# Optimization experiments

Hardware: AMD Instinct MI355X
Metric: run time of the kernel (lower is better)

The kernel has to match this reference:

```python
import jax, jax.numpy as jnp
import numpy as np

B, S, H, E, V = 64, 2048, 1024, 512, 32000


def setup_inputs() -> dict:
    key = jax.random.key(0)
    ks = jax.random.split(key, 10)
    s = lambda k, shape, scale: jax.random.normal(k, shape, jnp.float32) * scale
    return {
        "input_batch": jax.random.randint(ks[0], (B,), 0, V),
        "prev_h": s(ks[1], (B, H), 0.1),
        "prev_c": s(ks[2], (B, H), 0.1),
        "encoder_outputs": s(ks[3], (S, B, H), 0.1),
        "emb_W": s(ks[4], (V, E), 0.02),           # nn.Embedding weight
        "attn_W": s(ks[5], (2 * H,), 0.02),        # nn.Linear(2H, 1) weight (flattened)
        "attn_b": jnp.zeros((), jnp.float32),
        "W_ih": s(ks[6], (4 * H, E + H), 0.02),    # LSTMCell weight_ih
        "W_hh": s(ks[7], (4 * H, H), 0.02),        # LSTMCell weight_hh
        "b_ih": jnp.zeros((4 * H,), jnp.float32),
        "b_hh": jnp.zeros((4 * H,), jnp.float32),
        "out_W": s(ks[8], (V, H), 0.02),           # linear_out weight
        "out_b": jnp.zeros((V,), jnp.float32),
    }


def reference(input_batch, prev_h, prev_c, encoder_outputs, emb_W, attn_W, attn_b,
              W_ih, W_hh, b_ih, b_hh, out_W, out_b):
    hid = prev_h.shape[1]
    emb = emb_W[input_batch]                                   # [B, E]

    # Additive attention score attn(cat(prev_h[i], enc[j,i])) vectorized:
    # score[b, s] = prev_h[b] . W[:H] + enc[s, b] . W[H:] + bias
    Wh, We = attn_W[:hid], attn_W[hid:]
    scores = (prev_h @ Wh)[:, None] + jnp.einsum("sbh,h->bs", encoder_outputs, We) + attn_b
    attn_weights = jax.nn.softmax(scores, axis=1)              # [B, S]

    # context = bmm(attn[B,1,S], enc^T[B,S,H]) -> [B, H]
    context = jnp.einsum("bs,sbh->bh", attn_weights, encoder_outputs)

    x = jnp.concatenate([emb, context], axis=1)                # [B, E+H]

    # LSTMCell step (PyTorch gate order: i, f, g, o)
    gates = x @ W_ih.T + b_ih + prev_h @ W_hh.T + b_hh         # [B, 4H]
    i, f, g, o = jnp.split(gates, 4, axis=1)
    i, f, o = jax.nn.sigmoid(i), jax.nn.sigmoid(f), jax.nn.sigmoid(o)
    g = jnp.tanh(g)
    cell = f * prev_c + i * g
    hidden = o * jnp.tanh(cell)

    logits = hidden @ out_W.T + out_b                          # [B, V]
    output = jax.nn.log_softmax(logits, axis=1)
    return output, hidden, cell, attn_weights
```

## Files before the change

### kernel.cpp

```cpp
#include <hip/hip_runtime.h>
#include <math.h>

#define B 64
#define S 2048
#define H 1024
#define E 512
#define V 32000
#define G4 4096
#define KX 1536
#define KC 2560
#define NVT 500

typedef __attribute__((ext_vector_type(8))) short short8v;
typedef __attribute__((ext_vector_type(4))) float f32x4;

__device__ __forceinline__ ushort f2bf(float f) {
    union { float f; unsigned u; } v; v.f = f;
    unsigned r = v.u + 0x7FFFu + ((v.u >> 16) & 1u);
    return (ushort)(r >> 16);
}

__device__ __forceinline__ float4 ntload4(const float* p) {
    f32x4 v = __builtin_nontemporal_load((const f32x4*)p);
    return make_float4(v[0], v[1], v[2], v[3]);
}

__global__ __launch_bounds__(256) void prep_kernel(const int* __restrict__ ib,
                                                   const float* __restrict__ emb_W,
                                                   const float* __restrict__ prev_h,
                                                   const float* __restrict__ attn_W,
                                                   float* __restrict__ hwh,
                                                   float* __restrict__ xT) {
    __shared__ float red[256];
    int t = threadIdx.x;
    if (blockIdx.x < 64) {
        int b = blockIdx.x;
        float4 p = *(const float4*)(prev_h + b * H + t * 4);
        float4 w = *(const float4*)(attn_W + t * 4);
        red[t] = p.x * w.x + p.y * w.y + p.z * w.z + p.w * w.w;
        __syncthreads();
        for (int s2 = 128; s2; s2 >>= 1) {
            if (t < s2) red[t] += red[t + s2];
            __syncthreads();
        }
        if (t == 0) hwh[b] = red[0];
    } else {
        int g = (blockIdx.x - 64) * 256 + t;
        if (g < E * B) {
            int b = g & 63, k = g >> 6;
            xT[k * B + b] = emb_W[(size_t)ib[b] * E + k];
        } else {
            int g2 = g - E * B;
            int b = g2 & 63, k = g2 >> 6;
            xT[(KX + k) * B + b] = prev_h[b * H + k];
        }
    }
}

__global__ __launch_bounds__(256) void fused_attn_kernel(const float* __restrict__ enc,
                                                         const float* __restrict__ attn_W,
                                                         const float* __restrict__ attn_b,
                                                         const float* __restrict__ hwh,
                                                         float* __restrict__ scores,
                                                         float* __restrict__ cpart,
                                                         float* __restrict__ mlc) {
    __shared__ float mw[4], lw[4];
    __shared__ float cbuf[4][1024];
    int t = threadIdx.x;
    int lane = t & 63, wid = t >> 6;
    int bx = blockIdx.x;
    int b = bx >> 5, chunk = bx & 31;
    int s0 = chunk * 64 + wid * 16;

    const float* We = attn_W + H;
    float4 we4[4];
#pragma unroll
    for (int c = 0; c < 4; ++c) we4[c] = *(const float4*)(We + c * 256 + lane * 4);
    float cst = hwh[b] + attn_b[0];

    float m = -INFINITY, l = 0.f;
    float4 ctx4[4] = {{0,0,0,0},{0,0,0,0},{0,0,0,0},{0,0,0,0}};

    const float* rowp = enc + (size_t)s0 * (B * H) + b * H + lane * 4;
    float4 e4[4];
#pragma unroll
    for (int c = 0; c < 4; ++c) e4[c] = ntload4(rowp + c * 256);

    for (int i = 0; i < 16; ++i) {
        float4 cur[4];
#pragma unroll
        for (int c = 0; c < 4; ++c) cur[c] = e4[c];
        if (i < 15) {
            const float* np = rowp + (size_t)(i + 1) * (B * H);
#pragma unroll
            for (int c = 0; c < 4; ++c) e4[c] = ntload4(np + c * 256);
        }
        float acc = 0.f;
#pragma unroll
        for (int c = 0; c < 4; ++c)
            acc += cur[c].x * we4[c].x + cur[c].y * we4[c].y +
                   cur[c].z * we4[c].z + cur[c].w * we4[c].w;
#pragma unroll
        for (int x = 32; x; x >>= 1) acc += __shfl_xor(acc, x);
        float score = acc + cst;
        if (lane == 0) scores[b * S + s0 + i] = score;
        float nm = fmaxf(m, score);
        float sc = expf(m - nm);
        float w = expf(score - nm);
        l = l * sc + w;
        m = nm;
#pragma unroll
        for (int c = 0; c < 4; ++c) {
            ctx4[c].x = ctx4[c].x * sc + w * cur[c].x;
            ctx4[c].y = ctx4[c].y * sc + w * cur[c].y;
            ctx4[c].z = ctx4[c].z * sc + w * cur[c].z;
            ctx4[c].w = ctx4[c].w * sc + w * cur[c].w;
        }
    }

    if (lane == 0) { mw[wid] = m; lw[wid] = l; }
    __syncthreads();
    float M = fmaxf(fmaxf(mw[0], mw[1]), fmaxf(mw[2], mw[3]));
    float L = lw[0] * expf(mw[0] - M) + lw[1] * expf(mw[1] - M) +
              lw[2] * expf(mw[2] - M) + lw[3] * expf(mw[3] - M);
    float msc = expf(m - M);
#pragma unroll
    for (int c = 0; c < 4; ++c) {
        float4 v = ctx4[c];
        v.x *= msc; v.y *= msc; v.z *= msc; v.w *= msc;
        *(float4*)&cbuf[wid][c * 256 + lane * 4] = v;
    }
    __syncthreads();
    if (wid == 0) {
#pragma unroll
        for (int c = 0; c < 4; ++c) {
            int h = c * 256 + lane * 4;
            float4 a0 = *(float4*)&cbuf[0][h];
            float4 a1 = *(float4*)&cbuf[1][h];
            float4 a2 = *(float4*)&cbuf[2][h];
            float4 a3 = *(float4*)&cbuf[3][h];
            float4 s4 = make_float4(a0.x + a1.x + a2.x + a3.x,
                                    a0.y + a1.y + a2.y + a3.y,
                                    a0.z + a1.z + a2.z + a3.z,
                                    a0.w + a1.w + a2.w + a3.w);
            *(float4*)(cpart + (size_t)(chunk * B + b) * H + h) = s4;
        }
    }
    if (t == 0) {
        mlc[(b * 32 + chunk) * 2] = M;
        mlc[(b * 32 + chunk) * 2 + 1] = L;
    }
}

__global__ __launch_bounds__(256) void attn_reduce_kernel(const float* __restrict__ cpart,
                                                          const float* __restrict__ mlc,
                                                          const float* __restrict__ scores,
                                                          float* __restrict__ xT,
                                                          float* __restrict__ attn) {
    __shared__ float Ms[32], Ls[32], Es[32];
    int blk = blockIdx.x;
    int b = blk >> 2, q = blk & 3;
    int t = threadIdx.x;
    if (t < 32) {
        Ms[t] = mlc[(b * 32 + t) * 2];
        Ls[t] = mlc[(b * 32 + t) * 2 + 1];
    }
    __syncthreads();
    float Mg = -INFINITY;
#pragma unroll
    for (int c = 0; c < 32; ++c) Mg = fmaxf(Mg, Ms[c]);
    if (t < 32) Es[t] = expf(Ms[t] - Mg);
    __syncthreads();
    float Lg = 0.f;
#pragma unroll
    for (int c = 0; c < 32; ++c) Lg += Ls[c] * Es[c];
    float inv = 1.f / Lg;
    int h = q * 256 + t;
    float acc = 0.f;
#pragma unroll 4
    for (int c = 0; c < 32; ++c)
        acc += Es[c] * cpart[(size_t)(c * B + b) * H + h];
    xT[(E + h) * B + b] = acc * inv;
#pragma unroll
    for (int i = 0; i < 2; ++i) {
        int s = q * 512 + i * 256 + t;
        attn[b * S + s] = expf(scores[b * S + s] - Mg) * inv;
    }
}

__global__ __launch_bounds__(256) void gates_gemm(const float* __restrict__ W_ih,
                                                  const float* __restrict__ W_hh,
                                                  const float* __restrict__ xT,
                                                  float* __restrict__ gpart) {
    __shared__ float Wt[64][68];
    __shared__ float Xt[64][68];
    int t = threadIdx.x;
    int rtile = blockIdx.x >> 3, ks = blockIdx.x & 7;
    int r0 = rtile * 64;
    int rr0 = (t >> 4) * 4;
    int c0 = (t & 15) * 4;
    int sv = t >> 4;
    int sk = (t & 15) * 4;
    float acc[4][4] = {{0.f}};
    for (int kt = 0; kt < 5; ++kt) {
        int kb = ks * 320 + kt * 64;
        const float* wbase;
        int wstride;
        if (kb < KX) { wbase = W_ih + kb; wstride = KX; }
        else         { wbase = W_hh + (kb - KX); wstride = H; }
        __syncthreads();
#pragma unroll
        for (int g = 0; g < 4; ++g) {
            int vv = sv + g * 16;
            *(float4*)&Wt[vv][sk] = *(const float4*)(wbase + (size_t)(r0 + vv) * wstride + sk);
            *(float4*)&Xt[vv][sk] = *(const float4*)(xT + (size_t)(kb + vv) * B + sk);
        }
        __syncthreads();
#pragma unroll
        for (int k0 = 0; k0 < 64; k0 += 4) {
            float w[4][4], x[4][4];
#pragma unroll
            for (int ri = 0; ri < 4; ++ri) *(float4*)w[ri] = *(const float4*)&Wt[rr0 + ri][k0];
#pragma unroll
            for (int kj = 0; kj < 4; ++kj) *(float4*)x[kj] = *(const float4*)&Xt[k0 + kj][c0];
#pragma unroll
            for (int kj = 0; kj < 4; ++kj)
#pragma unroll
                for (int ri = 0; ri < 4; ++ri)
#pragma unroll
                    for (int ci = 0; ci < 4; ++ci)
                        acc[ri][ci] += w[ri][kj] * x[kj][ci];
        }
    }
#pragma unroll
    for (int ri = 0; ri < 4; ++ri) {
        float4 o4 = make_float4(acc[ri][0], acc[ri][1], acc[ri][2], acc[ri][3]);
        *(float4*)(gpart + (size_t)ks * (G4 * B) + (size_t)(r0 + rr0 + ri) * B + c0) = o4;
    }
}

__global__ __launch_bounds__(256) void lstm_kernel(const float* __restrict__ gpart,
                                                   const float* __restrict__ b_ih,
                                                   const float* __restrict__ b_hh,
                                                   const float* __restrict__ prev_c,
                                                   float* __restrict__ hidden_out,
                                                   float* __restrict__ cell_out,
                                                   ushort* __restrict__ hb) {
    int t = blockIdx.x * 256 + threadIdx.x;
    int b = t & 63, h = t >> 6;
    float g[4];
#pragma unroll
    for (int q = 0; q < 4; ++q) {
        int r = h + q * H;
        float a = b_ih[r] + b_hh[r];
#pragma unroll
        for (int ks = 0; ks < 8; ++ks) a += gpart[(size_t)ks * (G4 * B) + r * B + b];
        g[q] = a;
    }
    float ig = 1.f / (1.f + expf(-g[0]));
    float fg = 1.f / (1.f + expf(-g[1]));
    float gg = tanhf(g[2]);
    float og = 1.f / (1.f + expf(-g[3]));
    float c = fg * prev_c[b * H + h] + ig * gg;
    float hd = og * tanhf(c);
    cell_out[b * H + h] = c;
    hidden_out[b * H + h] = hd;
    hb[b * H + h] = f2bf(hd);
}

__global__ __launch_bounds__(256) void logits_mfma(const float* __restrict__ W,
                                                   const float* __restrict__ ob,
                                                   const ushort* __restrict__ hb,
                                                   float* __restrict__ outl,
                                                   float* __restrict__ lsp) {
    __shared__ ushort Wt[64 * 64];
    __shared__ ushort Bt[64 * 64];
    __shared__ float  Ct[64][68];
    int t = threadIdx.x;
    int lane = t & 63, wid = t >> 6;
    int v0 = blockIdx.x * 64;

    int srow = t >> 2;
    int sq = t & 3;

    f32x4 acc[4] = {{0.f,0.f,0.f,0.f},{0.f,0.f,0.f,0.f},{0.f,0.f,0.f,0.f},{0.f,0.f,0.f,0.f}};

    int r = lane & 15, g = lane >> 4;
    int arow = wid * 16 + r;
    int aswz = (arow & 7) << 4;
    unsigned abase = arow * 128;

    for (int kt = 0; kt < 16; ++kt) {
        int k0 = kt * 64;
        __syncthreads();
        {
            const float* src = W + (size_t)(v0 + srow) * H + k0 + sq * 16;
            float4 f0 = ntload4(src + 0);
            float4 f1 = ntload4(src + 4);
            float4 f2 = ntload4(src + 8);
            float4 f3 = ntload4(src + 12);
            short8v w0, w1;
            w0[0] = (short)f2bf(f0.x); w0[1] = (short)f2bf(f0.y);
            w0[2] = (short)f2bf(f0.z); w0[3] = (short)f2bf(f0.w);
            w0[4] = (short)f2bf(f1.x); w0[5] = (short)f2bf(f1.y);
            w0[6] = (short)f2bf(f1.z); w0[7] = (short)f2bf(f1.w);
            w1[0] = (short)f2bf(f2.x); w1[1] = (short)f2bf(f2.y);
            w1[2] = (short)f2bf(f2.z); w1[3] = (short)f2bf(f2.w);
            w1[4] = (short)f2bf(f3.x); w1[5] = (short)f2bf(f3.y);
            w1[6] = (short)f2bf(f3.z); w1[7] = (short)f2bf(f3.w);
            unsigned rb = srow * 128;
            unsigned sw = (srow & 7) << 4;
            *(short8v*)((char*)Wt + rb + ((sq * 32 + 0) ^ sw))  = w0;
            *(short8v*)((char*)Wt + rb + ((sq * 32 + 16) ^ sw)) = w1;
        }
        {
            const ushort* hsrc = hb + (size_t)srow * H + k0 + sq * 16;
            uint4 h0 = *(const uint4*)(hsrc);
            uint4 h1 = *(const uint4*)(hsrc + 8);
            unsigned rb = srow * 128;
            unsigned sw = (srow & 7) << 4;
            *(uint4*)((char*)Bt + rb + ((sq * 32 + 0) ^ sw))  = h0;
            *(uint4*)((char*)Bt + rb + ((sq * 32 + 16) ^ sw)) = h1;
        }
        __syncthreads();
#pragma unroll
        for (int kk = 0; kk < 2; ++kk) {
            unsigned koff = kk * 64 + g * 16;
            short8v a = *(short8v*)((char*)Wt + abase + (koff ^ aswz));
#pragma unroll
            for (int bt = 0; bt < 4; ++bt) {
                int brow = bt * 16 + r;
                short8v bb = *(short8v*)((char*)Bt + brow * 128 + (koff ^ ((brow & 7) << 4)));
                acc[bt] = __builtin_amdgcn_mfma_f32_16x16x32_bf16(a, bb, acc[bt], 0, 0, 0);
            }
        }
    }
    __syncthreads();
    float bias[4];
#pragma unroll
    for (int j = 0; j < 4; ++j) bias[j] = ob[v0 + wid * 16 + g * 4 + j];
#pragma unroll
    for (int bt = 0; bt < 4; ++bt)
#pragma unroll
        for (int j = 0; j < 4; ++j)
            Ct[bt * 16 + r][wid * 16 + g * 4 + j] = acc[bt][j] + bias[j];
    __syncthreads();
    int ob_ = t >> 2;
    int vq = (t & 3) * 16;
    float4 vals[4];
    float pm = -3.4e38f;
#pragma unroll
    for (int c = 0; c < 4; ++c) {
        vals[c] = *(float4*)&Ct[ob_][vq + c * 4];
        pm = fmaxf(pm, fmaxf(fmaxf(vals[c].x, vals[c].y), fmaxf(vals[c].z, vals[c].w)));
        *(float4*)(outl + (size_t)ob_ * V + v0 + vq + c * 4) = vals[c];
    }
    float ps = 0.f;
#pragma unroll
    for (int c = 0; c < 4; ++c)
        ps += expf(vals[c].x - pm) + expf(vals[c].y - pm) +
              expf(vals[c].z - pm) + expf(vals[c].w - pm);
#pragma unroll
    for (int x = 1; x <= 2; x <<= 1) {
        float om = __shfl_xor(pm, x);
        float os = __shfl_xor(ps, x);
        float nm = fmaxf(pm, om);
        ps = ps * expf(pm - nm) + os * expf(om - nm);
        pm = nm;
    }
    if ((t & 3) == 0) {
        lsp[((size_t)ob_ * NVT + blockIdx.x) * 2]     = pm;
        lsp[((size_t)ob_ * NVT + blockIdx.x) * 2 + 1] = ps;
    }
}

__global__ __launch_bounds__(256) void lsub_kernel(const float* __restrict__ lsp,
                                                   float* __restrict__ lg) {
    __shared__ float rm[256], rl[256];
    int blk = blockIdx.x;
    int b = blk >> 5, chunk = blk & 31;
    int t = threadIdx.x;
    const float* pb = lsp + (size_t)b * (NVT * 2);
    float m = pb[t * 2], l = pb[t * 2 + 1];
    int i2 = t + 256;
    if (i2 < NVT) {
        float m1 = pb[i2 * 2], l1 = pb[i2 * 2 + 1];
        float nm = fmaxf(m, m1);
        l = l * expf(m - nm) + l1 * expf(m1 - nm);
        m = nm;
    }
    rm[t] = m; rl[t] = l; __syncthreads();
    for (int s2 = 128; s2; s2 >>= 1) {
        if (t < s2) {
            float m2 = rm[t + s2], l2 = rl[t + s2];
            float nm = fmaxf(rm[t], m2);
            rl[t] = rl[t] * expf(rm[t] - nm) + l2 * expf(m2 - nm);
            rm[t] = nm;
        }
        __syncthreads();
    }
    float c = rm[0] + logf(rl[0]);
    if (t < 250) {
        float4* p = (float4*)(lg + (size_t)b * V + chunk * 1000) + t;
        float4 x = *p;
        x.x -= c; x.y -= c; x.z -= c; x.w -= c;
        *p = x;
    }
}

extern "C" void kernel_launch(void* const* d_in, const int* in_sizes, int n_in,
                              void* d_out, int out_size, void* d_ws, size_t ws_size,
                              hipStream_t stream) {
    const int*   ib      = (const int*)d_in[0];
    const float* prev_h  = (const float*)d_in[1];
    const float* prev_c  = (const float*)d_in[2];
    const float* enc     = (const float*)d_in[3];
    const float* emb_W   = (const float*)d_in[4];
    const float* attn_W  = (const float*)d_in[5];
    const float* attn_b  = (const float*)d_in[6];
    const float* W_ih    = (const float*)d_in[7];
    const float* W_hh    = (const float*)d_in[8];
    const float* b_ih    = (const float*)d_in[9];
    const float* b_hh    = (const float*)d_in[10];
    const float* out_W   = (const float*)d_in[11];
    const float* out_b   = (const float*)d_in[12];

    float* ws = (float*)d_ws;
    float* sc   = ws;
    float* hwh  = ws + 131072;
    float* xT   = ws + 131200;
    float* cp   = ws + 295040;
    float* gp   = cp;
    float* mlc  = ws + 2392192;
    ushort* hb  = (ushort*)(ws + 2396288);
    float* lsp  = ws + 2429056;

    float* out    = (float*)d_out;
    float* out_ls = out;
    float* out_h  = out + (size_t)B * V;
    float* out_c  = out_h + (size_t)B * H;
    float* out_a  = out_c + (size_t)B * H;

    hipLaunchKernelGGL(prep_kernel,        dim3(448),  dim3(256), 0, stream, ib, emb_W, prev_h, attn_W, hwh, xT);
    hipLaunchKernelGGL(fused_attn_kernel,  dim3(2048), dim3(256), 0, stream, enc, attn_W, attn_b, hwh, sc, cp, mlc);
    hipLaunchKernelGGL(attn_reduce_kernel, dim3(256),  dim3(256), 0, stream, cp, mlc, sc, xT, out_a);
    hipLaunchKernelGGL(gates_gemm,         dim3(512),  dim3(256), 0, stream, W_ih, W_hh, xT, gp);
    hipLaunchKernelGGL(lstm_kernel,        dim3(256),  dim3(256), 0, stream, gp, b_ih, b_hh, prev_c, out_h, out_c, hb);
    hipLaunchKernelGGL(logits_mfma,        dim3(NVT),  dim3(256), 0, stream, out_W, out_b, hb, out_ls, lsp);
    hipLaunchKernelGGL(lsub_kernel,        dim3(2048), dim3(256), 0, stream, lsp, out_ls);
}
```

Measured before the change: 184.3 us.

## Fold prep into attention, use bf16 MFMA for gates GEMM

Removes the separate prep kernel. The prev_h·Wh dot product now runs inside each attention block, and the x-vector gather moves into attn_reduce, which writes a bf16 row-major buffer. The attention grid is halved so each block handles two chunks, which halves the partial context and the reduce work. The fp32 FMA gates GEMM is replaced by a bf16 MFMA kernel that converts weights on the fly into swizzled LDS. This trades gates precision and some attention parallelism for fewer launches and faster matrix math.

```diff
diff --git a/kernel.cpp b/kernel.cpp
--- a/kernel.cpp
+++ b/kernel.cpp
@@ -25,96 +25,78 @@
     return make_float4(v[0], v[1], v[2], v[3]);
 }
 
-__global__ __launch_bounds__(256) void prep_kernel(const int* __restrict__ ib,
-                                                   const float* __restrict__ emb_W,
-                                                   const float* __restrict__ prev_h,
-                                                   const float* __restrict__ attn_W,
-                                                   float* __restrict__ hwh,
-                                                   float* __restrict__ xT) {
-    __shared__ float red[256];
-    int t = threadIdx.x;
-    if (blockIdx.x < 64) {
-        int b = blockIdx.x;
-        float4 p = *(const float4*)(prev_h + b * H + t * 4);
-        float4 w = *(const float4*)(attn_W + t * 4);
-        red[t] = p.x * w.x + p.y * w.y + p.z * w.z + p.w * w.w;
-        __syncthreads();
-        for (int s2 = 128; s2; s2 >>= 1) {
-            if (t < s2) red[t] += red[t + s2];
-            __syncthreads();
-        }
-        if (t == 0) hwh[b] = red[0];
-    } else {
-        int g = (blockIdx.x - 64) * 256 + t;
-        if (g < E * B) {
-            int b = g & 63, k = g >> 6;
-            xT[k * B + b] = emb_W[(size_t)ib[b] * E + k];
-        } else {
-            int g2 = g - E * B;
-            int b = g2 & 63, k = g2 >> 6;
-            xT[(KX + k) * B + b] = prev_h[b * H + k];
-        }
-    }
-}
-
 __global__ __launch_bounds__(256) void fused_attn_kernel(const float* __restrict__ enc,
                                                          const float* __restrict__ attn_W,
                                                          const float* __restrict__ attn_b,
-                                                         const float* __restrict__ hwh,
+                                                         const float* __restrict__ prev_h,
                                                          float* __restrict__ scores,
                                                          float* __restrict__ cpart,
                                                          float* __restrict__ mlc) {
+    __shared__ float red[256];
     __shared__ float mw[4], lw[4];
     __shared__ float cbuf[4][1024];
     int t = threadIdx.x;
     int lane = t & 63, wid = t >> 6;
-    int bx = blockIdx.x;
-    int b = bx >> 5, chunk = bx & 31;
-    int s0 = chunk * 64 + wid * 16;
+    int b = blockIdx.x >> 4, cpair = blockIdx.x & 15;
+
+    {
+        float4 p = *(const float4*)(prev_h + b * H + t * 4);
+        float4 w = *(const float4*)(attn_W + t * 4);
+        red[t] = p.x * w.x + p.y * w.y + p.z * w.z + p.w * w.w;
+        __syncthreads();
+        for (int s2 = 128; s2; s2 >>= 1) {
+            if (t < s2) red[t] += red[t + s2];
+            __syncthreads();
+        }
+    }
+    float cst = red[0] + attn_b[0];
 
     const float* We = attn_W + H;
     float4 we4[4];
 #pragma unroll
     for (int c = 0; c < 4; ++c) we4[c] = *(const float4*)(We + c * 256 + lane * 4);
-    float cst = hwh[b] + attn_b[0];
 
     float m = -INFINITY, l = 0.f;
     float4 ctx4[4] = {{0,0,0,0},{0,0,0,0},{0,0,0,0},{0,0,0,0}};
 
-    const float* rowp = enc + (size_t)s0 * (B * H) + b * H + lane * 4;
-    float4 e4[4];
-#pragma unroll
-    for (int c = 0; c < 4; ++c) e4[c] = ntload4(rowp + c * 256);
-
-    for (int i = 0; i < 16; ++i) {
-        float4 cur[4];
-#pragma unroll
-        for (int c = 0; c < 4; ++c) cur[c] = e4[c];
-        if (i < 15) {
-            const float* np = rowp + (size_t)(i + 1) * (B * H);
-#pragma unroll
-            for (int c = 0; c < 4; ++c) e4[c] = ntload4(np + c * 256);
-        }
-        float acc = 0.f;
-#pragma unroll
-        for (int c = 0; c < 4; ++c)
-            acc += cur[c].x * we4[c].x + cur[c].y * we4[c].y +
-                   cur[c].z * we4[c].z + cur[c].w * we4[c].w;
-#pragma unroll
-        for (int x = 32; x; x >>= 1) acc += __shfl_xor(acc, x);
-        float score = acc + cst;
-        if (lane == 0) scores[b * S + s0 + i] = score;
-        float nm = fmaxf(m, score);
-        float sc = expf(m - nm);
-        float w = expf(score - nm);
-        l = l * sc + w;
-        m = nm;
-#pragma unroll
-        for (int c = 0; c < 4; ++c) {
-            ctx4[c].x = ctx4[c].x * sc + w * cur[c].x;
-            ctx4[c].y = ctx4[c].y * sc + w * cur[c].y;
-            ctx4[c].z = ctx4[c].z * sc + w * cur[c].z;
-            ctx4[c].w = ctx4[c].w * sc + w * cur[c].w;
+    for (int cc = 0; cc < 2; ++cc) {
+        int chunk = cpair * 2 + cc;
+        int s0 = chunk * 64 + wid * 16;
+        const float* rowp = enc + (size_t)s0 * (B * H) + b * H + lane * 4;
+        float4 e4[4];
+#pragma unroll
+        for (int c = 0; c < 4; ++c) e4[c] = ntload4(rowp + c * 256);
+
+        for (int i = 0; i < 16; ++i) {
+            float4 cur[4];
+#pragma unroll
+            for (int c = 0; c < 4; ++c) cur[c] = e4[c];
+            if (i < 15) {
+                const float* np = rowp + (size_t)(i + 1) * (B * H);
+#pragma unroll
+                for (int c = 0; c < 4; ++c) e4[c] = ntload4(np + c * 256);
+            }
+            float acc = 0.f;
+#pragma unroll
+            for (int c = 0; c < 4; ++c)
+                acc += cur[c].x * we4[c].x + cur[c].y * we4[c].y +
+                       cur[c].z * we4[c].z + cur[c].w * we4[c].w;
+#pragma unroll
+            for (int x = 32; x; x >>= 1) acc += __shfl_xor(acc, x);
+            float score = acc + cst;
+            if (lane == 0) scores[b * S + s0 + i] = score;
+            float nm = fmaxf(m, score);
+            float sc = expf(m - nm);
+            float w = expf(score - nm);
+            l = l * sc + w;
+            m = nm;
+#pragma unroll
+            for (int c = 0; c < 4; ++c) {
+                ctx4[c].x = ctx4[c].x * sc + w * cur[c].x;
+                ctx4[c].y = ctx4[c].y * sc + w * cur[c].y;
+                ctx4[c].z = ctx4[c].z * sc + w * cur[c].z;
+                ctx4[c].w = ctx4[c].w * sc + w * cur[c].w;
+            }
         }
     }
 
@@ -143,65 +125,82 @@
                                     a0.y + a1.y + a2.y + a3.y,
                                     a0.z + a1.z + a2.z + a3.z,
                                     a0.w + a1.w + a2.w + a3.w);
-            *(float4*)(cpart + (size_t)(chunk * B + b) * H + h) = s4;
+            *(float4*)(cpart + (size_t)(cpair * B + b) * H + h) = s4;
         }
     }
     if (t == 0) {
-        mlc[(b * 32 + chunk) * 2] = M;
-        mlc[(b * 32 + chunk) * 2 + 1] = L;
+        mlc[(b * 16 + cpair) * 2] = M;
+        mlc[(b * 16 + cpair) * 2 + 1] = L;
     }
 }
 
 __global__ __launch_bounds__(256) void attn_reduce_kernel(const float* __restrict__ cpart,
                                                           const float* __restrict__ mlc,
                                                           const float* __restrict__ scores,
-                                                          float* __restrict__ xT,
+                                                          const int* __restrict__ ib,
+                                                          const float* __restrict__ emb_W,
+                                                          const float* __restrict__ prev_h,
+                                                          ushort* __restrict__ xb,
                                                           float* __restrict__ attn) {
-    __shared__ float Ms[32], Ls[32], Es[32];
+    __shared__ float Ms[16], Ls[16], Es[16];
     int blk = blockIdx.x;
     int b = blk >> 2, q = blk & 3;
     int t = threadIdx.x;
-    if (t < 32) {
-        Ms[t] = mlc[(b * 32 + t) * 2];
-        Ls[t] = mlc[(b * 32 + t) * 2 + 1];
+    if (t < 16) {
+        Ms[t] = mlc[(b * 16 + t) * 2];
+        Ls[t] = mlc[(b * 16 + t) * 2 + 1];
     }
     __syncthreads();
     float Mg = -INFINITY;
 #pragma unroll
-    for (int c = 0; c < 32; ++c) Mg = fmaxf(Mg, Ms[c]);
-    if (t < 32) Es[t] = expf(Ms[t] - Mg);
+    for (int c = 0; c < 16; ++c) Mg = fmaxf(Mg, Ms[c]);
+    if (t < 16) Es[t] = expf(Ms[t] - Mg);
     __syncthreads();
     float Lg = 0.f;
 #pragma unroll
-    for (int c = 0; c < 32; ++c) Lg += Ls[c] * Es[c];
+    for (int c = 0; c < 16; ++c) Lg += Ls[c] * Es[c];
     float inv = 1.f / Lg;
     int h = q * 256 + t;
     float acc = 0.f;
 #pragma unroll 4
-    for (int c = 0; c < 32; ++c)
+    for (int c = 0; c < 16; ++c)
         acc += Es[c] * cpart[(size_t)(c * B + b) * H + h];
-    xT[(E + h) * B + b] = acc * inv;
+    xb[(size_t)b * KC + E + h] = f2bf(acc * inv);
 #pragma unroll
     for (int i = 0; i < 2; ++i) {
         int s = q * 512 + i * 256 + t;
         attn[b * S + s] = expf(scores[b * S + s] - Mg) * inv;
     }
-}
-
-__global__ __launch_bounds__(256) void gates_gemm(const float* __restrict__ W_ih,
+#pragma unroll
+    for (int i = 0; i < 2; ++i) {
+        int j = q * 384 + i * 256 + t;
+        if (i == 1 && t >= 128) break;
+        if (j < E) xb[(size_t)b * KC + j] = f2bf(emb_W[(size_t)ib[b] * E + j]);
+        else       xb[(size_t)b * KC + KX + (j - E)] = f2bf(prev_h[b * H + (j - E)]);
+    }
+}
+
+__global__ __launch_bounds__(256) void gates_mfma(const float* __restrict__ W_ih,
                                                   const float* __restrict__ W_hh,
-                                                  const float* __restrict__ xT,
+                                                  const ushort* __restrict__ xb,
                                                   float* __restrict__ gpart) {
-    __shared__ float Wt[64][68];
-    __shared__ float Xt[64][68];
+    __shared__ ushort Wt[64 * 64];
+    __shared__ ushort Bt[64 * 64];
     int t = threadIdx.x;
+    int lane = t & 63, wid = t >> 6;
     int rtile = blockIdx.x >> 3, ks = blockIdx.x & 7;
     int r0 = rtile * 64;
-    int rr0 = (t >> 4) * 4;
-    int c0 = (t & 15) * 4;
-    int sv = t >> 4;
-    int sk = (t & 15) * 4;
-    float acc[4][4] = {{0.f}};
+
+    int srow = t >> 2;
+    int sq = t & 3;
+
+    f32x4 acc[4] = {{0.f,0.f,0.f,0.f},{0.f,0.f,0.f,0.f},{0.f,0.f,0.f,0.f},{0.f,0.f,0.f,0.f}};
+
+    int r = lane & 15, g = lane >> 4;
+    int arow = wid * 16 + r;
+    int aswz = (arow & 7) << 4;
+    unsigned abase = arow * 128;
+
     for (int kt = 0; kt < 5; ++kt) {
         int kb = ks * 320 + kt * 64;
         const float* wbase;
@@ -209,33 +208,56 @@
         if (kb < KX) { wbase = W_ih + kb; wstride = KX; }
         else         { wbase = W_hh + (kb - KX); wstride = H; }
         __syncthreads();
-#pragma unroll
-        for (int g = 0; g < 4; ++g) {
-            int vv = sv + g * 16;
-            *(float4*)&Wt[vv][sk] = *(const float4*)(wbase + (size_t)(r0 + vv) * wstride + sk);
-            *(float4*)&Xt[vv][sk] = *(const float4*)(xT + (size_t)(kb + vv) * B + sk);
-        }
-        __syncthreads();
-#pragma unroll
-        for (int k0 = 0; k0 < 64; k0 += 4) {
-            float w[4][4], x[4][4];
-#pragma unroll
-            for (int ri = 0; ri < 4; ++ri) *(float4*)w[ri] = *(const float4*)&Wt[rr0 + ri][k0];
-#pragma unroll
-            for (int kj = 0; kj < 4; ++kj) *(float4*)x[kj] = *(const float4*)&Xt[k0 + kj][c0];
-#pragma unroll
-            for (int kj = 0; kj < 4; ++kj)
-#pragma unroll
-                for (int ri = 0; ri < 4; ++ri)
-#pragma unroll
-                    for (int ci = 0; ci < 4; ++ci)
-                        acc[ri][ci] += w[ri][kj] * x[kj][ci];
-        }
-    }
-#pragma unroll
-    for (int ri = 0; ri < 4; ++ri) {
-        float4 o4 = make_float4(acc[ri][0], acc[ri][1], acc[ri][2], acc[ri][3]);
-        *(float4*)(gpart + (size_t)ks * (G4 * B) + (size_t)(r0 + rr0 + ri) * B + c0) = o4;
+        {
+            const float* src = wbase + (size_t)(r0 + srow) * wstride + sq * 16;
+            float4 f0 = ntload4(src + 0);
+            float4 f1 = ntload4(src + 4);
+            float4 f2 = ntload4(src + 8);
+            float4 f3 = ntload4(src + 12);
+            short8v w0, w1;
+            w0[0] = (short)f2bf(f0.x); w0[1] = (short)f2bf(f0.y);
+            w0[2] = (short)f2bf(f0.z); w0[3] = (short)f2bf(f0.w);
+            w0[4] = (short)f2bf(f1.x); w0[5] = (short)f2bf(f1.y);
+            w0[6] = (short)f2bf(f1.z); w0[7] = (short)f2bf(f1.w);
+            w1[0] = (short)f2bf(f2.x); w1[1] = (short)f2bf(f2.y);
+            w1[2] = (short)f2bf(f2.z); w1[3] = (short)f2bf(f2.w);
+            w1[4] = (short)f2bf(f3.x); w1[5] = (short)f2bf(f3.y);
+            w1[6] = (short)f2bf(f3.z); w1[7] = (short)f2bf(f3.w);
+            unsigned rb = srow * 128;
+            unsigned sw = (srow & 7) << 4;
+            *(short8v*)((char*)Wt + rb + ((sq * 32 + 0) ^ sw))  = w0;
+            *(short8v*)((char*)Wt + rb + ((sq * 32 + 16) ^ sw)) = w1;
+        }
+        {
+            const ushort* hsrc = xb + (size_t)srow * KC + kb + sq * 16;
+            uint4 h0 = *(const uint4*)(hsrc);
+            uint4 h1 = *(const uint4*)(hsrc + 8);
+            unsigned rb = srow * 128;
+            unsigned sw = (srow & 7) << 4;
+            *(uint4*)((char*)Bt + rb + ((sq * 32 + 0) ^ sw))  = h0;
+            *(uint4*)((char*)Bt + rb + ((sq * 32 + 16) ^ sw)) = h1;
+        }
+        __syncthreads();
+#pragma unroll
+        for (int kk = 0; kk < 2; ++kk) {
+            unsigned koff = kk * 64 + g * 16;
+            short8v a = *(short8v*)((char*)Wt + abase + (koff ^ aswz));
+#pragma unroll
+            for (int bt = 0; bt < 4; ++bt) {
+                int brow = bt * 16 + r;
+                short8v bb = *(short8v*)((char*)Bt + brow * 128 + (koff ^ ((brow & 7) << 4)));
+                acc[bt] = __builtin_amdgcn_mfma_f32_16x16x32_bf16(a, bb, acc[bt], 0, 0, 0);
+            }
+        }
+    }
+#pragma unroll
+    for (int bt = 0; bt < 4; ++bt) {
+        int bcol = bt * 16 + r;
+#pragma unroll
+        for (int j = 0; j < 4; ++j) {
+            int rg = r0 + wid * 16 + g * 4 + j;
+            gpart[(size_t)ks * (G4 * B) + (size_t)rg * B + bcol] = acc[bt][j];
+        }
     }
 }
 
@@ -427,13 +449,12 @@
 
     float* ws = (float*)d_ws;
     float* sc   = ws;
-    float* hwh  = ws + 131072;
-    float* xT   = ws + 131200;
-    float* cp   = ws + 295040;
-    float* gp   = cp;
-    float* mlc  = ws + 2392192;
-    ushort* hb  = (ushort*)(ws + 2396288);
-    float* lsp  = ws + 2429056;
+    float* cp   = ws + 131072;
+    float* gp   = ws + 1179648;
+    float* mlc  = ws + 3276800;
+    ushort* xb  = (ushort*)(ws + 3278848);
+    ushort* hb  = (ushort*)(ws + 3360768);
+    float* lsp  = ws + 3393536;
 
     float* out    = (float*)d_out;
     float* out_ls = out;
@@ -441,10 +462,9 @@
     float* out_c  = out_h + (size_t)B * H;
     float* out_a  = out_c + (size_t)B * H;
 
-    hipLaunchKernelGGL(prep_kernel,        dim3(448),  dim3(256), 0, stream, ib, emb_W, prev_h, attn_W, hwh, xT);
-    hipLaunchKernelGGL(fused_attn_kernel,  dim3(2048), dim3(256), 0, stream, enc, attn_W, attn_b, hwh, sc, cp, mlc);
-    hipLaunchKernelGGL(attn_reduce_kernel, dim3(256),  dim3(256), 0, stream, cp, mlc, sc, xT, out_a);
-    hipLaunchKernelGGL(gates_gemm,         dim3(512),  dim3(256), 0, stream, W_ih, W_hh, xT, gp);
+    hipLaunchKernelGGL(fused_attn_kernel,  dim3(1024), dim3(256), 0, stream, enc, attn_W, attn_b, prev_h, sc, cp, mlc);
+    hipLaunchKernelGGL(attn_reduce_kernel, dim3(256),  dim3(256), 0, stream, cp, mlc, sc, ib, emb_W, prev_h, xb, out_a);
+    hipLaunchKernelGGL(gates_mfma,         dim3(512),  dim3(256), 0, stream, W_ih, W_hh, xb, gp);
     hipLaunchKernelGGL(lstm_kernel,        dim3(256),  dim3(256), 0, stream, gp, b_ih, b_hh, prev_c, out_h, out_c, hb);
     hipLaunchKernelGGL(logits_mfma,        dim3(NVT),  dim3(256), 0, stream, out_W, out_b, hb, out_ls, lsp);
     hipLaunchKernelGGL(lsub_kernel,        dim3(2048), dim3(256), 0, stream, lsp, out_ls);
```

Measured after the change: 168.6 us. -8.5%, faster.
